# Performance work log

Hardware: AMD Instinct MI355X
Metric: run time of the kernel (lower is better)

## Reference

```python
import jax, jax.numpy as jnp
import numpy as np

B, H, S, DK, DV = 2, 16, 2048, 64, 64


def setup_inputs() -> dict:
    key = jax.random.key(0)
    kq, kk, kv, km = jax.random.split(key, 4)
    Q = jax.random.normal(kq, (B, H, S, DK), dtype=jnp.float32)
    K = jax.random.normal(kk, (B, H, S, DK), dtype=jnp.float32)
    V = jax.random.normal(kv, (B, H, S, DV), dtype=jnp.float32)
    attn_mask = jax.random.randint(km, (B, H, S, S), 0, 2).astype(jnp.bool_)
    return {
        "Q": Q, "K": K, "V": V, "attn_mask": attn_mask,
        "d_model": 1024, "n_layers": 6, "n_heads": H,
        "d_k": DK, "d_v": DV, "d_ff": 4096,
    }


def reference(Q, K, V, attn_mask, d_model, n_layers, n_heads, d_k, d_v, d_ff):
    # scores: [B, H, S, S] = Q K^T / sqrt(d_k)
    scale = 1.0 / np.sqrt(d_k).astype(np.float32)
    scores = jnp.einsum('bhqd,bhkd->bhqk', Q, K) * scale
    scores = jnp.where(attn_mask, jnp.asarray(-1e9, scores.dtype), scores)
    attn = jax.nn.softmax(scores, axis=-1)
    context = jnp.einsum('bhqk,bhkd->bhqd', attn, V)
    return (context, attn)
```

## Files before the change

kernel.cpp:

```cpp
#include <hip/hip_runtime.h>
#include <hip/hip_fp16.h>

#define S_LEN 2048
#define DKV 64
#define NBH 32
#define CTX_ELEMS ((size_t)NBH * S_LEN * DKV)

using half8 = __attribute__((ext_vector_type(8))) _Float16;
using half4 = __attribute__((ext_vector_type(4))) _Float16;
using f32x4 = __attribute__((ext_vector_type(4))) float;
using u32x4 = __attribute__((ext_vector_type(4))) unsigned int;

#define MFMA16x32(a, b, c) __builtin_amdgcn_mfma_f32_16x16x32_f16((a), (b), (c), 0, 0, 0)

__global__ void detect_mask_kernel(const unsigned char* __restrict__ mask,
                                   int* __restrict__ flag) {
  __shared__ int nz0s, nzos;
  if (threadIdx.x == 0) { nz0s = 0; nzos = 0; }
  __syncthreads();
  int nz0 = 0, nzo = 0;
  for (int i = threadIdx.x; i < 65536; i += 256) {
    unsigned char b = mask[i];
    if (b) { if ((i & 3) == 0) nz0++; else nzo++; }
  }
  atomicAdd(&nz0s, nz0);
  atomicAdd(&nzos, nzo);
  __syncthreads();
  if (threadIdx.x == 0) *flag = (nz0s > 0 && nzos > 0) ? 0 : 1;
}

__global__ void pack_mask_kernel(const void* __restrict__ maskv,
                                 const int* __restrict__ flag,
                                 unsigned int* __restrict__ bits) {
  __shared__ unsigned char nib[256];
  const bool w4 = (*flag) != 0;
  const unsigned int* m32 = (const unsigned int*)maskv;
  const int tid = threadIdx.x;
  for (int it = 0; it < 64; ++it) {
    const size_t e0 = ((size_t)blockIdx.x * 64 + it) * 1024;
    const size_t ei = e0 + (size_t)tid * 4;
    unsigned int nv;
    if (w4) {
      u32x4 v = __builtin_nontemporal_load((const u32x4*)(m32 + ei));
      nv = (v[0] ? 1u : 0u) | (v[1] ? 2u : 0u) | (v[2] ? 4u : 0u) | (v[3] ? 8u : 0u);
    } else {
      unsigned int b = __builtin_nontemporal_load(m32 + (ei >> 2));
      nv = ((b & 0xffu) ? 1u : 0u) | ((b & 0xff00u) ? 2u : 0u) |
           ((b & 0xff0000u) ? 4u : 0u) | ((b & 0xff000000u) ? 8u : 0u);
    }
    __syncthreads();
    nib[tid] = (unsigned char)nv;
    __syncthreads();
    if (tid < 32) {
      unsigned int dw = 0;
#pragma unroll
      for (int t = 0; t < 8; ++t)
        dw |= ((unsigned int)nib[tid * 8 + t]) << (t * 4);
      bits[(e0 >> 5) + tid] = dw;
    }
  }
}

__global__ void convert_f32_f16_kernel(const float* __restrict__ src,
                                       _Float16* __restrict__ dst) {
  size_t i = (size_t)blockIdx.x * blockDim.x + threadIdx.x;
  f32x4 v = *(const f32x4*)(src + i * 4);
  half4 h;
#pragma unroll
  for (int j = 0; j < 4; j++) h[j] = (_Float16)v[j];
  *(half4*)(dst + i * 4) = h;
}

__global__ void transpose_v_kernel(const float* __restrict__ V,
                                   _Float16* __restrict__ VT) {
  __shared__ _Float16 t[64][68];
  const int bh = blockIdx.y;
  const int k0 = blockIdx.x * 64;
  const float* Vb = V + ((size_t)bh * S_LEN + k0) * DKV;
#pragma unroll
  for (int it = 0; it < 4; it++) {
    int idx = threadIdx.x + it * 256;
    int kl = idx >> 4;
    int dq = (idx & 15) * 4;
    f32x4 v = *(const f32x4*)(Vb + (size_t)kl * DKV + dq);
#pragma unroll
    for (int j = 0; j < 4; j++) t[kl][dq + j] = (_Float16)v[j];
  }
  __syncthreads();
  _Float16* VTb = VT + (size_t)bh * DKV * S_LEN;
#pragma unroll
  for (int it = 0; it < 4; it++) {
    int idx = threadIdx.x + it * 256;
    int d = idx >> 4;
    int kq = (idx & 15) * 4;
    half4 h;
#pragma unroll
    for (int j = 0; j < 4; j++) h[j] = t[kq + j][d];
    *(half4*)(VTb + (size_t)d * S_LEN + k0 + kq) = h;
  }
}

__global__ __launch_bounds__(512, 2)
void attn_v7_kernel(const _Float16* __restrict__ QH, const _Float16* __restrict__ KH,
                    const _Float16* __restrict__ VT, const unsigned int* __restrict__ bits,
                    float* __restrict__ out) {
  __shared__ __align__(16) _Float16 pbuf[8][32][40];
  __shared__ float zbuf[4][2][32];
  __shared__ __align__(16) float cbuf[4][32][64];

  const int tid = threadIdx.x;
  const int w = tid >> 6;
  const int lane = tid & 63;
  const int g = lane >> 4;
  const int c = lane & 15;
  const int tb = w >> 1;
  const int half = w & 1;

  const int phys = blockIdx.x;
  const int orig = (phys & 7) * 64 + (phys >> 3);
  const int tile = orig * 4 + tb;
  const int bh = tile >> 6;
  const int q0 = (tile & 63) << 5;

  const _Float16* qpA = QH + ((size_t)(bh * S_LEN + q0 + c)) * DKV + g * 8;
  const half8 aA0 = *(const half8*)qpA;
  const half8 aA1 = *(const half8*)(qpA + 32);
  const _Float16* qpB = qpA + 16 * DKV;
  const half8 aB0 = *(const half8*)qpB;
  const half8 aB1 = *(const half8*)(qpB + 32);

  const _Float16* Kb = KH + (size_t)bh * S_LEN * DKV;
  const unsigned int* bq = bits + ((size_t)(bh * S_LEN + q0)) * (S_LEN / 32);

  float ZsA[4] = {0.0f, 0.0f, 0.0f, 0.0f};
  float ZsB[4] = {0.0f, 0.0f, 0.0f, 0.0f};

  for (int kt4 = half * 8; kt4 < half * 8 + 8; ++kt4) {
#pragma unroll
    for (int sub = 0; sub < 4; ++sub) {
      const int kt = kt4 * 4 + sub;
      unsigned int mwA[4], mwB[4];
#pragma unroll
      for (int e = 0; e < 4; e++) {
        mwA[e] = bq[(size_t)(g * 4 + e) * (S_LEN / 32) + kt];
        mwB[e] = bq[(size_t)(16 + g * 4 + e) * (S_LEN / 32) + kt];
      }
      const _Float16* kp = Kb + ((size_t)(kt * 32 + c)) * DKV + g * 8;
      half8 k00 = *(const half8*)kp;
      half8 k01 = *(const half8*)(kp + 32);
      half8 k10 = *(const half8*)(kp + 16 * DKV);
      half8 k11 = *(const half8*)(kp + 16 * DKV + 32);
      f32x4 acA0 = (f32x4)0.0f, acA1 = (f32x4)0.0f;
      f32x4 acB0 = (f32x4)0.0f, acB1 = (f32x4)0.0f;
      acA0 = MFMA16x32(aA0, k00, acA0);
      acA0 = MFMA16x32(aA1, k01, acA0);
      acB0 = MFMA16x32(aB0, k00, acB0);
      acB0 = MFMA16x32(aB1, k01, acB0);
      acA1 = MFMA16x32(aA0, k10, acA1);
      acA1 = MFMA16x32(aA1, k11, acA1);
      acB1 = MFMA16x32(aB0, k10, acB1);
      acB1 = MFMA16x32(aB1, k11, acB1);
#pragma unroll
      for (int e = 0; e < 4; e++) {
        float pA0 = ((mwA[e] >> c) & 1u) ? 0.0f : __expf(acA0[e] * 0.125f);
        float pA1 = ((mwA[e] >> (16 + c)) & 1u) ? 0.0f : __expf(acA1[e] * 0.125f);
        float pB0 = ((mwB[e] >> c) & 1u) ? 0.0f : __expf(acB0[e] * 0.125f);
        float pB1 = ((mwB[e] >> (16 + c)) & 1u) ? 0.0f : __expf(acB1[e] * 0.125f);
        ZsA[e] += pA0 + pA1;
        ZsB[e] += pB0 + pB1;
      }
    }
  }
#pragma unroll
  for (int off = 1; off < 16; off <<= 1) {
#pragma unroll
    for (int e = 0; e < 4; e++) {
      ZsA[e] += __shfl_xor(ZsA[e], off, 64);
      ZsB[e] += __shfl_xor(ZsB[e], off, 64);
    }
  }
  if (c == 0) {
#pragma unroll
    for (int e = 0; e < 4; e++) {
      zbuf[tb][half][g * 4 + e] = ZsA[e];
      zbuf[tb][half][16 + g * 4 + e] = ZsB[e];
    }
  }
  __syncthreads();
  float lZA[4], lZB[4];
#pragma unroll
  for (int e = 0; e < 4; e++) {
    lZA[e] = __logf(zbuf[tb][0][g * 4 + e] + zbuf[tb][1][g * 4 + e]);
    lZB[e] = __logf(zbuf[tb][0][16 + g * 4 + e] + zbuf[tb][1][16 + g * 4 + e]);
  }

  f32x4 ctxA[4], ctxB[4];
#pragma unroll
  for (int nn = 0; nn < 4; nn++) { ctxA[nn] = (f32x4)0.0f; ctxB[nn] = (f32x4)0.0f; }

  const _Float16* Vb = VT + (size_t)bh * DKV * S_LEN;
  float* attn_base = out + CTX_ELEMS + ((size_t)(bh * S_LEN + q0)) * S_LEN;

  for (int kt4 = half * 8; kt4 < half * 8 + 8; ++kt4) {
#pragma unroll
    for (int sub = 0; sub < 4; ++sub) {
      const int kt = kt4 * 4 + sub;
      unsigned int mwA[4], mwB[4];
#pragma unroll
      for (int e = 0; e < 4; e++) {
        mwA[e] = bq[(size_t)(g * 4 + e) * (S_LEN / 32) + kt];
        mwB[e] = bq[(size_t)(16 + g * 4 + e) * (S_LEN / 32) + kt];
      }
      const _Float16* kp = Kb + ((size_t)(kt * 32 + c)) * DKV + g * 8;
      half8 k00 = *(const half8*)kp;
      half8 k01 = *(const half8*)(kp + 32);
      half8 k10 = *(const half8*)(kp + 16 * DKV);
      half8 k11 = *(const half8*)(kp + 16 * DKV + 32);
      f32x4 acA0 = (f32x4)0.0f, acA1 = (f32x4)0.0f;
      f32x4 acB0 = (f32x4)0.0f, acB1 = (f32x4)0.0f;
      acA0 = MFMA16x32(aA0, k00, acA0);
      acA0 = MFMA16x32(aA1, k01, acA0);
      acB0 = MFMA16x32(aB0, k00, acB0);
      acB0 = MFMA16x32(aB1, k01, acB0);
      acA1 = MFMA16x32(aA0, k10, acA1);
      acA1 = MFMA16x32(aA1, k11, acA1);
      acB1 = MFMA16x32(aB0, k10, acB1);
      acB1 = MFMA16x32(aB1, k11, acB1);
#pragma unroll
      for (int e = 0; e < 4; e++) {
        float pA0 = ((mwA[e] >> c) & 1u) ? 0.0f : __expf(acA0[e] * 0.125f - lZA[e]);
        float pA1 = ((mwA[e] >> (16 + c)) & 1u) ? 0.0f : __expf(acA1[e] * 0.125f - lZA[e]);
        float pB0 = ((mwB[e] >> c) & 1u) ? 0.0f : __expf(acB0[e] * 0.125f - lZB[e]);
        float pB1 = ((mwB[e] >> (16 + c)) & 1u) ? 0.0f : __expf(acB1[e] * 0.125f - lZB[e]);
        pbuf[w][g * 4 + e][c] = (_Float16)pA0;
        pbuf[w][g * 4 + e][16 + c] = (_Float16)pA1;
        pbuf[w][16 + g * 4 + e][c] = (_Float16)pB0;
        pbuf[w][16 + g * 4 + e][16 + c] = (_Float16)pB1;
      }
      half8 paA = *(const half8*)&pbuf[w][c][g * 8];
      half8 paB = *(const half8*)&pbuf[w][16 + c][g * 8];

#pragma unroll
      for (int s = 0; s < 4; s++) {
        const int r = (lane >> 3) + s * 8;
        const int c4 = (lane & 7) * 4;
        half4 h = *(const half4*)&pbuf[w][r][c4];
        f32x4 o;
#pragma unroll
        for (int j = 0; j < 4; j++) o[j] = (float)h[j];
        __builtin_nontemporal_store(o,
            (f32x4*)(attn_base + (size_t)r * S_LEN + kt * 32 + c4));
      }
#pragma unroll
      for (int nn = 0; nn < 4; nn++) {
        const _Float16* vp = Vb + (size_t)(nn * 16 + c) * S_LEN + kt * 32 + g * 8;
        half8 vb = *(const half8*)vp;
        ctxA[nn] = MFMA16x32(paA, vb, ctxA[nn]);
        ctxB[nn] = MFMA16x32(paB, vb, ctxB[nn]);
      }
    }
  }

  __syncthreads();
  if (half == 1) {
#pragma unroll
    for (int nn = 0; nn < 4; nn++) {
#pragma unroll
      for (int e = 0; e < 4; e++) {
        cbuf[tb][g * 4 + e][nn * 16 + c] = ctxA[nn][e];
        cbuf[tb][16 + g * 4 + e][nn * 16 + c] = ctxB[nn][e];
      }
    }
  }
  __syncthreads();
  if (half == 0) {
    float* cb = out + ((size_t)(bh * S_LEN + q0)) * DKV;
#pragma unroll
    for (int nn = 0; nn < 4; nn++) {
#pragma unroll
      for (int e = 0; e < 4; e++) {
        float vA = ctxA[nn][e] + cbuf[tb][g * 4 + e][nn * 16 + c];
        float vB = ctxB[nn][e] + cbuf[tb][16 + g * 4 + e][nn * 16 + c];
        __builtin_nontemporal_store(vA, cb + (size_t)(g * 4 + e) * DKV + nn * 16 + c);
        __builtin_nontemporal_store(vB, cb + (size_t)(16 + g * 4 + e) * DKV + nn * 16 + c);
      }
    }
  }
}

__global__ __launch_bounds__(512, 1)
void attn_slow_kernel(const float* __restrict__ Q, const float* __restrict__ K,
                      const float* __restrict__ V, const void* __restrict__ maskv,
                      float* __restrict__ out, const int* __restrict__ flag) {
  __shared__ __align__(16) unsigned char smem[16 * 2056 * 2];
  __shared__ float redm[8][16];
  __shared__ float reds[8][16];
  _Float16 (*P)[2056] = (_Float16 (*)[2056])smem;

  const int bh = blockIdx.y;
  const int q0 = blockIdx.x << 4;
  const int tid = threadIdx.x;
  const int w = tid >> 6;
  const int lane = tid & 63;
  const int g = lane >> 4;
  const int c = lane & 15;
  const int k0 = w << 8;

  const bool mask_w = (*flag) != 0;
  const unsigned char* m8 = (const unsigned char*)maskv;
  const unsigned int* m32 = (const unsigned int*)maskv;

  const float* Qb = Q + ((size_t)bh * S_LEN + q0) * DKV;
  const float* Kb = K + (size_t)bh * S_LEN * DKV;
  const float* Vb = V + (size_t)bh * S_LEN * DKV;
  const size_t mbase = ((size_t)bh * S_LEN + q0) * S_LEN;
  float* ctx_out = out + ((size_t)bh * S_LEN + q0) * DKV;
  float* attn_out = out + CTX_ELEMS + mbase;

  half8 a0, a1;
  {
    const float* qrow = Qb + (size_t)c * DKV + g * 8;
    f32x4 x0 = *(const f32x4*)(qrow);
    f32x4 x1 = *(const f32x4*)(qrow + 4);
    f32x4 y0 = *(const f32x4*)(qrow + 32);
    f32x4 y1 = *(const f32x4*)(qrow + 36);
#pragma unroll
    for (int j = 0; j < 4; j++) {
      a0[j] = (_Float16)x0[j]; a0[4 + j] = (_Float16)x1[j];
      a1[j] = (_Float16)y0[j]; a1[4 + j] = (_Float16)y1[j];
    }
  }

  f32x4 acc[16];
#pragma unroll
  for (int n = 0; n < 16; n++) acc[n] = (f32x4)0.0f;
#pragma unroll
  for (int n = 0; n < 16; n++) {
    const float* kr = Kb + (size_t)(k0 + n * 16 + c) * DKV + g * 8;
    f32x4 x0 = *(const f32x4*)(kr);
    f32x4 x1 = *(const f32x4*)(kr + 4);
    f32x4 y0 = *(const f32x4*)(kr + 32);
    f32x4 y1 = *(const f32x4*)(kr + 36);
    half8 b0, b1;
#pragma unroll
    for (int j = 0; j < 4; j++) {
      b0[j] = (_Float16)x0[j]; b0[4 + j] = (_Float16)x1[j];
      b1[j] = (_Float16)y0[j]; b1[4 + j] = (_Float16)y1[j];
    }
    acc[n] = MFMA16x32(a0, b0, acc[n]);
    acc[n] = MFMA16x32(a1, b1, acc[n]);
  }

  float mx[4] = {-1e9f, -1e9f, -1e9f, -1e9f};
#pragma unroll
  for (int n = 0; n < 16; n++) {
    const int kc = k0 + n * 16 + c;
#pragma unroll
    for (int e = 0; e < 4; e++) {
      const size_t mi = mbase + (size_t)(g * 4 + e) * S_LEN + kc;
      bool masked;
      if (mask_w) masked = (__builtin_nontemporal_load(&m32[mi]) != 0u);
      else        masked = (__builtin_nontemporal_load(&m8[mi]) != 0);
      float s = masked ? -1e9f : acc[n][e] * 0.125f;
      acc[n][e] = s;
      mx[e] = fmaxf(mx[e], s);
    }
  }
#pragma unroll
  for (int off = 1; off < 16; off <<= 1) {
#pragma unroll
    for (int e = 0; e < 4; e++)
      mx[e] = fmaxf(mx[e], __shfl_xor(mx[e], off, 64));
  }
  if (c == 0) {
#pragma unroll
    for (int e = 0; e < 4; e++) redm[w][g * 4 + e] = mx[e];
  }
  __syncthreads();
  float m[4], sm[4];
#pragma unroll
  for (int e = 0; e < 4; e++) {
    float v = redm[0][g * 4 + e];
#pragma unroll
    for (int ww = 1; ww < 8; ww++) v = fmaxf(v, redm[ww][g * 4 + e]);
    m[e] = v;
    sm[e] = 0.0f;
  }
#pragma unroll
  for (int n = 0; n < 16; n++) {
#pragma unroll
    for (int e = 0; e < 4; e++) {
      float p = __expf(acc[n][e] - m[e]);
      acc[n][e] = p;
      sm[e] += p;
    }
  }
#pragma unroll
  for (int off = 1; off < 16; off <<= 1) {
#pragma unroll
    for (int e = 0; e < 4; e++) sm[e] += __shfl_xor(sm[e], off, 64);
  }
  if (c == 0) {
#pragma unroll
    for (int e = 0; e < 4; e++) reds[w][g * 4 + e] = sm[e];
  }
  __syncthreads();
  float inv[4];
#pragma unroll
  for (int e = 0; e < 4; e++) {
    float z = 0.0f;
#pragma unroll
    for (int ww = 0; ww < 8; ww++) z += reds[ww][g * 4 + e];
    inv[e] = 1.0f / z;
  }
#pragma unroll
  for (int n = 0; n < 16; n++) {
    const int kc = k0 + n * 16 + c;
#pragma unroll
    for (int e = 0; e < 4; e++) {
      float v = acc[n][e] * inv[e];
      __builtin_nontemporal_store(v, &attn_out[(size_t)(g * 4 + e) * S_LEN + kc]);
      P[g * 4 + e][kc] = (_Float16)v;
    }
  }
  __syncthreads();

  f32x4 ctx[4];
#pragma unroll
  for (int n = 0; n < 4; n++) ctx[n] = (f32x4)0.0f;
  for (int ks = 0; ks < 8; ks++) {
    const int kb = k0 + ks * 32;
    half8 pa = *(const half8*)&P[c][kb + g * 8];
#pragma unroll
    for (int n = 0; n < 4; n++) {
      const float* vp = Vb + (size_t)(kb + g * 8) * DKV + n * 16 + c;
      half8 vb;
#pragma unroll
      for (int j = 0; j < 8; j++) vb[j] = (_Float16)vp[(size_t)j * DKV];
      ctx[n] = MFMA16x32(pa, vb, ctx[n]);
    }
  }
  __syncthreads();

  float* red2 = (float*)smem;
#pragma unroll
  for (int n = 0; n < 4; n++) {
#pragma unroll
    for (int e = 0; e < 4; e++)
      red2[((w * 16) + g * 4 + e) * 64 + n * 16 + c] = ctx[n][e];
  }
  __syncthreads();
  for (int i = tid; i < 16 * 64; i += 512) {
    int q = i >> 6, d = i & 63;
    float ssum = 0.0f;
#pragma unroll
    for (int ww = 0; ww < 8; ww++) ssum += red2[((ww * 16) + q) * 64 + d];
    ctx_out[(size_t)q * DKV + d] = ssum;
  }
}

extern "C" void kernel_launch(void* const* d_in, const int* in_sizes, int n_in,
                              void* d_out, int out_size, void* d_ws, size_t ws_size,
                              hipStream_t stream) {
  (void)in_sizes; (void)n_in; (void)out_size;
  const float* Q = (const float*)d_in[0];
  const float* K = (const float*)d_in[1];
  const float* V = (const float*)d_in[2];
  const void* mask = d_in[3];

  const size_t HBYTES = (size_t)NBH * S_LEN * DKV * sizeof(_Float16);
  const size_t BITBYTES = (size_t)NBH * S_LEN * (S_LEN / 32) * 4;
  const size_t NEED = 256 + 3 * HBYTES + BITBYTES;

  int* flag = (int*)d_ws;
  hipLaunchKernelGGL(detect_mask_kernel, dim3(1), dim3(256), 0, stream,
                     (const unsigned char*)mask, flag);

  if (ws_size >= NEED) {
    _Float16* QH = (_Float16*)((char*)d_ws + 256);
    _Float16* KH = (_Float16*)((char*)d_ws + 256 + HBYTES);
    _Float16* VT = (_Float16*)((char*)d_ws + 256 + 2 * HBYTES);
    unsigned int* bits = (unsigned int*)((char*)d_ws + 256 + 3 * HBYTES);
    const int n4 = NBH * S_LEN * DKV / 4;
    hipLaunchKernelGGL(pack_mask_kernel, dim3(2048), dim3(256), 0, stream,
                       mask, flag, bits);
    hipLaunchKernelGGL(convert_f32_f16_kernel, dim3(n4 / 256), dim3(256), 0, stream, Q, QH);
    hipLaunchKernelGGL(convert_f32_f16_kernel, dim3(n4 / 256), dim3(256), 0, stream, K, KH);
    hipLaunchKernelGGL(transpose_v_kernel, dim3(S_LEN / 64, NBH), dim3(256), 0, stream, V, VT);
    hipLaunchKernelGGL(attn_v7_kernel, dim3(512), dim3(512), 0, stream,
                       QH, KH, VT, bits, (float*)d_out);
  } else {
    hipLaunchKernelGGL(attn_slow_kernel, dim3(128, 32), dim3(512), 0, stream,
                       Q, K, V, mask, (float*)d_out, flag);
  }
}
```

Before: 385.7 us.

## Ballot-pack mask, fold softmax scale into Q, store attn directly from registers

The mask packer's 4-byte-bool path now builds bits with a wavefront ballot, which removes the shared-memory nibble staging and two barriers per iteration. The 1/sqrt(d_k) factor is applied during the Q fp16 conversion, so the per-element multiply leaves the attention inner loops. The attention probabilities are written straight from fp32 registers as scalar nontemporal stores instead of being read back from the fp16 LDS buffer, which also makes the stored attn full precision rather than fp16-rounded. pbuf and cbuf now share one LDS allocation to cut shared-memory use, at the cost of more, narrower (4-byte) global store instructions.

```diff
diff --git a/kernel.cpp b/kernel.cpp
--- a/kernel.cpp
+++ b/kernel.cpp
@@ -34,40 +34,47 @@
                                  unsigned int* __restrict__ bits) {
   __shared__ unsigned char nib[256];
   const bool w4 = (*flag) != 0;
-  const unsigned int* m32 = (const unsigned int*)maskv;
   const int tid = threadIdx.x;
-  for (int it = 0; it < 64; ++it) {
-    const size_t e0 = ((size_t)blockIdx.x * 64 + it) * 1024;
-    const size_t ei = e0 + (size_t)tid * 4;
-    unsigned int nv;
-    if (w4) {
-      u32x4 v = __builtin_nontemporal_load((const u32x4*)(m32 + ei));
-      nv = (v[0] ? 1u : 0u) | (v[1] ? 2u : 0u) | (v[2] ? 4u : 0u) | (v[3] ? 8u : 0u);
-    } else {
+  if (w4) {
+    const unsigned int* m32 = (const unsigned int*)maskv;
+    const int w = tid >> 6;
+    const int lane = tid & 63;
+    size_t base = ((size_t)blockIdx.x * 4 + w) * (256 * 64);
+    for (int i = 0; i < 256; ++i) {
+      unsigned int v = __builtin_nontemporal_load(m32 + base + lane);
+      unsigned long long b = __ballot(v != 0u);
+      if (lane < 2) bits[(base >> 5) + lane] = (unsigned int)(b >> (lane * 32));
+      base += 64;
+    }
+  } else {
+    const unsigned int* m32 = (const unsigned int*)maskv;
+    for (int it = 0; it < 64; ++it) {
+      const size_t e0 = ((size_t)blockIdx.x * 64 + it) * 1024;
+      const size_t ei = e0 + (size_t)tid * 4;
       unsigned int b = __builtin_nontemporal_load(m32 + (ei >> 2));
-      nv = ((b & 0xffu) ? 1u : 0u) | ((b & 0xff00u) ? 2u : 0u) |
-           ((b & 0xff0000u) ? 4u : 0u) | ((b & 0xff000000u) ? 8u : 0u);
-    }
-    __syncthreads();
-    nib[tid] = (unsigned char)nv;
-    __syncthreads();
-    if (tid < 32) {
-      unsigned int dw = 0;
-#pragma unroll
-      for (int t = 0; t < 8; ++t)
-        dw |= ((unsigned int)nib[tid * 8 + t]) << (t * 4);
-      bits[(e0 >> 5) + tid] = dw;
+      unsigned int nv = ((b & 0xffu) ? 1u : 0u) | ((b & 0xff00u) ? 2u : 0u) |
+                        ((b & 0xff0000u) ? 4u : 0u) | ((b & 0xff000000u) ? 8u : 0u);
+      __syncthreads();
+      nib[tid] = (unsigned char)nv;
+      __syncthreads();
+      if (tid < 32) {
+        unsigned int dw = 0;
+#pragma unroll
+        for (int t = 0; t < 8; ++t)
+          dw |= ((unsigned int)nib[tid * 8 + t]) << (t * 4);
+        bits[(e0 >> 5) + tid] = dw;
+      }
     }
   }
 }
 
 __global__ void convert_f32_f16_kernel(const float* __restrict__ src,
-                                       _Float16* __restrict__ dst) {
+                                       _Float16* __restrict__ dst, float scale) {
   size_t i = (size_t)blockIdx.x * blockDim.x + threadIdx.x;
   f32x4 v = *(const f32x4*)(src + i * 4);
   half4 h;
 #pragma unroll
-  for (int j = 0; j < 4; j++) h[j] = (_Float16)v[j];
+  for (int j = 0; j < 4; j++) h[j] = (_Float16)(v[j] * scale);
   *(half4*)(dst + i * 4) = h;
 }
 
@@ -101,12 +108,13 @@
 }
 
 __global__ __launch_bounds__(512, 2)
-void attn_v7_kernel(const _Float16* __restrict__ QH, const _Float16* __restrict__ KH,
+void attn_v8_kernel(const _Float16* __restrict__ QH, const _Float16* __restrict__ KH,
                     const _Float16* __restrict__ VT, const unsigned int* __restrict__ bits,
                     float* __restrict__ out) {
-  __shared__ __align__(16) _Float16 pbuf[8][32][40];
+  __shared__ __align__(16) unsigned char smem[32768];
   __shared__ float zbuf[4][2][32];
-  __shared__ __align__(16) float cbuf[4][32][64];
+  _Float16 (*pbuf)[32][40] = (_Float16 (*)[32][40])smem;
+  float (*cbuf)[32][64] = (float (*)[32][64])smem;
 
   const int tid = threadIdx.x;
   const int w = tid >> 6;
@@ -162,10 +170,10 @@
       acB1 = MFMA16x32(aB1, k11, acB1);
 #pragma unroll
       for (int e = 0; e < 4; e++) {
-        float pA0 = ((mwA[e] >> c) & 1u) ? 0.0f : __expf(acA0[e] * 0.125f);
-        float pA1 = ((mwA[e] >> (16 + c)) & 1u) ? 0.0f : __expf(acA1[e] * 0.125f);
-        float pB0 = ((mwB[e] >> c) & 1u) ? 0.0f : __expf(acB0[e] * 0.125f);
-        float pB1 = ((mwB[e] >> (16 + c)) & 1u) ? 0.0f : __expf(acB1[e] * 0.125f);
+        float pA0 = ((mwA[e] >> c) & 1u) ? 0.0f : __expf(acA0[e]);
+        float pA1 = ((mwA[e] >> (16 + c)) & 1u) ? 0.0f : __expf(acA1[e]);
+        float pB0 = ((mwB[e] >> c) & 1u) ? 0.0f : __expf(acB0[e]);
+        float pB1 = ((mwB[e] >> (16 + c)) & 1u) ? 0.0f : __expf(acB1[e]);
         ZsA[e] += pA0 + pA1;
         ZsB[e] += pB0 + pB1;
       }
@@ -226,31 +234,26 @@
       acA1 = MFMA16x32(aA1, k11, acA1);
       acB1 = MFMA16x32(aB0, k10, acB1);
       acB1 = MFMA16x32(aB1, k11, acB1);
+
+      float* ab = attn_base + kt * 32 + c;
 #pragma unroll
       for (int e = 0; e < 4; e++) {
-        float pA0 = ((mwA[e] >> c) & 1u) ? 0.0f : __expf(acA0[e] * 0.125f - lZA[e]);
-        float pA1 = ((mwA[e] >> (16 + c)) & 1u) ? 0.0f : __expf(acA1[e] * 0.125f - lZA[e]);
-        float pB0 = ((mwB[e] >> c) & 1u) ? 0.0f : __expf(acB0[e] * 0.125f - lZB[e]);
-        float pB1 = ((mwB[e] >> (16 + c)) & 1u) ? 0.0f : __expf(acB1[e] * 0.125f - lZB[e]);
+        float pA0 = ((mwA[e] >> c) & 1u) ? 0.0f : __expf(acA0[e] - lZA[e]);
+        float pA1 = ((mwA[e] >> (16 + c)) & 1u) ? 0.0f : __expf(acA1[e] - lZA[e]);
+        float pB0 = ((mwB[e] >> c) & 1u) ? 0.0f : __expf(acB0[e] - lZB[e]);
+        float pB1 = ((mwB[e] >> (16 + c)) & 1u) ? 0.0f : __expf(acB1[e] - lZB[e]);
         pbuf[w][g * 4 + e][c] = (_Float16)pA0;
         pbuf[w][g * 4 + e][16 + c] = (_Float16)pA1;
         pbuf[w][16 + g * 4 + e][c] = (_Float16)pB0;
         pbuf[w][16 + g * 4 + e][16 + c] = (_Float16)pB1;
+        __builtin_nontemporal_store(pA0, ab + (size_t)(g * 4 + e) * S_LEN);
+        __builtin_nontemporal_store(pA1, ab + (size_t)(g * 4 + e) * S_LEN + 16);
+        __builtin_nontemporal_store(pB0, ab + (size_t)(16 + g * 4 + e) * S_LEN);
+        __builtin_nontemporal_store(pB1, ab + (size_t)(16 + g * 4 + e) * S_LEN + 16);
       }
       half8 paA = *(const half8*)&pbuf[w][c][g * 8];
       half8 paB = *(const half8*)&pbuf[w][16 + c][g * 8];
 
-#pragma unroll
-      for (int s = 0; s < 4; s++) {
-        const int r = (lane >> 3) + s * 8;
-        const int c4 = (lane & 7) * 4;
-        half4 h = *(const half4*)&pbuf[w][r][c4];
-        f32x4 o;
-#pragma unroll
-        for (int j = 0; j < 4; j++) o[j] = (float)h[j];
-        __builtin_nontemporal_store(o,
-            (f32x4*)(attn_base + (size_t)r * S_LEN + kt * 32 + c4));
-      }
 #pragma unroll
       for (int nn = 0; nn < 4; nn++) {
         const _Float16* vp = Vb + (size_t)(nn * 16 + c) * S_LEN + kt * 32 + g * 8;
@@ -484,10 +487,12 @@
     const int n4 = NBH * S_LEN * DKV / 4;
     hipLaunchKernelGGL(pack_mask_kernel, dim3(2048), dim3(256), 0, stream,
                        mask, flag, bits);
-    hipLaunchKernelGGL(convert_f32_f16_kernel, dim3(n4 / 256), dim3(256), 0, stream, Q, QH);
-    hipLaunchKernelGGL(convert_f32_f16_kernel, dim3(n4 / 256), dim3(256), 0, stream, K, KH);
+    hipLaunchKernelGGL(convert_f32_f16_kernel, dim3(n4 / 256), dim3(256), 0, stream,
+                       Q, QH, 0.125f);
+    hipLaunchKernelGGL(convert_f32_f16_kernel, dim3(n4 / 256), dim3(256), 0, stream,
+                       K, KH, 1.0f);
     hipLaunchKernelGGL(transpose_v_kernel, dim3(S_LEN / 64, NBH), dim3(256), 0, stream, V, VT);
-    hipLaunchKernelGGL(attn_v7_kernel, dim3(512), dim3(512), 0, stream,
+    hipLaunchKernelGGL(attn_v8_kernel, dim3(512), dim3(512), 0, stream,
                        QH, KH, VT, bits, (float*)d_out);
   } else {
     hipLaunchKernelGGL(attn_slow_kernel, dim3(128, 32), dim3(512), 0, stream,
```

New measurement: 449.7 us. +16.6%, slower.
